# Optimization experiments

Measured on AMD Instinct MI355X. Metric: run time of the kernel, lower is better.

## Reference

```python
import jax, jax.numpy as jnp
import numpy as np

HALF_STEP = 0.05
NUM_V = 10  # clamp(floor(0.5/0.05), 2, 1000)
EPS = 1e-6


def _normalize(x):
    return x / (jnp.linalg.norm(x, axis=-1, keepdims=True) + EPS)


def _ragged_structure(edge_points_np):
    # Concrete (numpy) ragged-grid index structure: per-edge horizontal sample
    # counts from edge length, exclusive-cumsum offsets, repeat_interleave ids.
    sp = edge_points_np[:, 0]
    cd = edge_points_np[:, 1] - sp
    cl = np.linalg.norm(cd + EPS, axis=1)
    num_h = np.clip((cl // HALF_STEP).astype(np.int64), 2, 1000)  # [N]
    total_x = int(num_h.sum())
    begin = np.concatenate([[0], np.cumsum(num_h)[:-1]])           # roll-based exclusive cumsum
    eid_x = np.repeat(np.arange(len(num_h)), num_h)                # [total_x] edge id per x-sample
    pos_x = np.arange(total_x) - begin[eid_x]                      # dx integer position within edge
    eid = np.repeat(eid_x, NUM_V)                                  # [P] edge id per sample point
    pos_x_full = np.repeat(pos_x, NUM_V).astype(np.float32)        # coords_x integer part
    dy_idx = np.tile(np.arange(NUM_V), total_x).astype(np.float32) # coords_y integer part
    denom_full = np.repeat((num_h - 1)[eid_x], NUM_V).astype(np.float32)
    return (jnp.asarray(eid), jnp.asarray(pos_x_full), jnp.asarray(denom_full),
            jnp.asarray(dy_idx))


def _sample_img(img, uv):
    # img [1,3,H,W]; uv [P,2] in [0,1) -> bilinear sample (align_corners style)
    im = img[0]
    H, W = im.shape[1], im.shape[2]
    x = uv[:, 0] * (W - 1)
    y = uv[:, 1] * (H - 1)
    x0 = jnp.floor(x).astype(jnp.int32)
    y0 = jnp.floor(y).astype(jnp.int32)
    x1 = jnp.clip(x0 + 1, 0, W - 1)
    y1 = jnp.clip(y0 + 1, 0, H - 1)
    wx = (x - x0)[None]
    wy = (y - y0)[None]
    g = lambda yy, xx: im[:, yy, xx]  # [3,P] gather
    out = (g(y0, x0) * (1 - wx) * (1 - wy) + g(y0, x1) * wx * (1 - wy)
           + g(y1, x0) * (1 - wx) * wy + g(y1, x1) * wx * wy)
    return out.T  # [P,3]


def _forward(edge_points, intrinsic1, intrinsic2, extrinsic1, extrinsic2,
             rgb1, rgb2, eid, pos_x, denom, dy_idx):
    start = edge_points[:, 0]
    cur_dir = edge_points[:, 1] - start
    next_dir = edge_points[:, 3] - edge_points[:, 1]
    prev_dir = edge_points[:, 0] - edge_points[:, 2]
    cur_len = jnp.linalg.norm(cur_dir + EPS, axis=1)
    cur_dir = cur_dir / cur_len[:, None]
    cur_normal = _normalize(jnp.cross(cur_dir, next_dir))
    flip = cur_normal[:, 2] > 0  # dot with (0,0,1) > 0 -> flip sign
    cur_normal = jnp.where(flip[:, None], -cur_normal, cur_normal)
    cur_up = _normalize(jnp.cross(cur_normal, cur_dir))
    prev_normal = _normalize(jnp.cross(prev_dir, cur_dir))

    # ragged per-edge sample grid (repeat_interleave realized via gather on eid)
    coords_x = pos_x / denom * cur_len[eid]          # [P]
    coords_y = dy_idx / (NUM_V - 1) * 0.5            # [P]
    pts = (cur_dir[eid] * coords_x[:, None]
           + cur_up[eid] * coords_y[:, None]
           + start[eid])                              # [P,3]

    # view 1 projection + bilinear sample
    uv1 = pts @ intrinsic1.T
    uv1 = jnp.clip(uv1[:, :2] / uv1[:, 2:3], 0.0, 0.999999)
    s1 = _sample_img(rgb1, uv1)

    # view 2: K2_homog @ E2 @ inv(E1) applied to homogeneous points
    K2h = jnp.eye(4, dtype=pts.dtype).at[:3, :3].set(intrinsic2)
    T = K2h @ extrinsic2 @ jnp.linalg.inv(extrinsic1)
    ph = jnp.concatenate([pts, jnp.ones_like(pts[:, :1])], axis=1)
    uv2 = ph @ T.T
    uv2 = jnp.clip(uv2[:, :2] / uv2[:, 2:3], 0.0, 0.999999)
    s2 = _sample_img(rgb2, uv2)

    similarity_loss = jnp.mean((s1 - s2) ** 2)
    normal_loss = jnp.mean(1.0 - jnp.sum(cur_normal * prev_normal, axis=1)) / 2.0
    obs_normal = _normalize(jnp.cross(edge_points[:, 0], edge_points[:, 1]))
    snp = jnp.minimum(jnp.abs(jnp.sum(cur_up * obs_normal, axis=1)), 0.5)
    normalization_loss = jnp.mean(1.0 - snp / 0.5)
    return jnp.stack([similarity_loss, normal_loss, normalization_loss])


def setup_inputs() -> dict:
    key = jax.random.key(0)
    k0, k1, k2 = jax.random.split(key, 3)
    N, H, W = 10000, 1500, 2000
    # camera-space edge endpoints/neighbors, pushed in front of the camera
    edge_points = jax.random.normal(k0, (N, 4, 3), dtype=jnp.float32) \
        + jnp.array([0.0, 0.0, 6.0], dtype=jnp.float32)
    intrinsic1 = jnp.array([[0.3, 0.0, 0.5], [0.0, 0.3, 0.5], [0.0, 0.0, 1.0]],
                           dtype=jnp.float32)
    intrinsic2 = intrinsic1
    extrinsic1 = jnp.eye(4, dtype=jnp.float32)
    extrinsic2 = jnp.eye(4, dtype=jnp.float32).at[:3, 3].set(
        jnp.array([0.1, 0.0, 0.0], dtype=jnp.float32))
    rgb1 = jax.random.uniform(k1, (1, 3, H, W), dtype=jnp.float32)
    rgb2 = jax.random.uniform(k2, (1, 3, H, W), dtype=jnp.float32)
    return {"edge_points": edge_points, "intrinsic1": intrinsic1,
            "intrinsic2": intrinsic2, "extrinsic1": extrinsic1,
            "extrinsic2": extrinsic2, "rgb1": rgb1, "rgb2": rgb2}


def reference(edge_points, intrinsic1, intrinsic2, extrinsic1, extrinsic2,
              rgb1, rgb2):
    eid, pos_x, denom, dy_idx = _ragged_structure(np.asarray(edge_points))
    return _forward(edge_points, intrinsic1, intrinsic2, extrinsic1,
                    extrinsic2, rgb1, rgb2, eid, pos_x, denom, dy_idx)
```

## Files before the change

### kernel.cpp

```cpp
#include <hip/hip_runtime.h>
#include <math.h>

#define EPSF 1e-6f
#define NUM_V 10
#define W_IMG 2000
#define H_IMG 1500
#define HW_IMG (W_IMG * H_IMG)
#define TH_QUAD (H_IMG - 1)
#define SAMPLE_BLOCKS 2048
#define MAX_CHUNKS 80

__device__ __forceinline__ void cross3(const float a[3], const float b[3], float c[3]) {
    c[0] = a[1] * b[2] - a[2] * b[1];
    c[1] = a[2] * b[0] - a[0] * b[2];
    c[2] = a[0] * b[1] - a[1] * b[0];
}
__device__ __forceinline__ float dot3(const float a[3], const float b[3]) {
    return a[0] * b[0] + a[1] * b[1] + a[2] * b[2];
}
__device__ __forceinline__ float norm3(const float a[3]) {
    return sqrtf(a[0] * a[0] + a[1] * a[1] + a[2] * a[2]);
}

__device__ void do_init(const float* __restrict__ K2, const float* __restrict__ E1,
                        const float* __restrict__ E2, float* __restrict__ T) {
    double M[4][8];
    for (int i = 0; i < 4; ++i)
        for (int j = 0; j < 4; ++j) {
            M[i][j] = (double)E1[i * 4 + j];
            M[i][j + 4] = (i == j) ? 1.0 : 0.0;
        }
    for (int col = 0; col < 4; ++col) {
        int piv = col;
        double best = fabs(M[col][col]);
        for (int r = col + 1; r < 4; ++r) {
            double v = fabs(M[r][col]);
            if (v > best) { best = v; piv = r; }
        }
        if (piv != col)
            for (int j = 0; j < 8; ++j) {
                double t = M[col][j]; M[col][j] = M[piv][j]; M[piv][j] = t;
            }
        double d = M[col][col];
        for (int j = 0; j < 8; ++j) M[col][j] /= d;
        for (int r = 0; r < 4; ++r) {
            if (r == col) continue;
            double f = M[r][col];
            for (int j = 0; j < 8; ++j) M[r][j] -= f * M[col][j];
        }
    }
    double E[4][4];
    for (int i = 0; i < 4; ++i)
        for (int j = 0; j < 4; ++j) {
            double s = 0.0;
            for (int k = 0; k < 4; ++k) s += (double)E2[i * 4 + k] * M[k][j + 4];
            E[i][j] = s;
        }
    for (int i = 0; i < 4; ++i)
        for (int j = 0; j < 4; ++j) {
            double s = 0.0;
            if (i < 3) {
                for (int k = 0; k < 3; ++k) s += (double)K2[i * 3 + k] * E[k][j];
            } else {
                s = E[3][j];
            }
            T[i * 4 + j] = (float)s;
        }
}

__global__ __launch_bounds__(256) void geom_kernel(const float* __restrict__ ep, int N,
                                                   float4* __restrict__ geo,
                                                   int* __restrict__ nwv,
                                                   double* __restrict__ gnl,
                                                   double* __restrict__ gzl,
                                                   double* __restrict__ gcnt) {
    const int e = blockIdx.x * 256 + threadIdx.x;
    float nl = 0.f, zl = 0.f;
    int cn = 0;
    if (e < N) {
        const float4* P4 = (const float4*)(ep + (size_t)e * 12);
        float4 a4 = P4[0], b4 = P4[1], c4 = P4[2];
        float p0[3] = {a4.x, a4.y, a4.z};
        float p1[3] = {a4.w, b4.x, b4.y};
        float p2[3] = {b4.z, b4.w, c4.x};
        float p3[3] = {c4.y, c4.z, c4.w};
        float cd[3] = {p1[0] - p0[0], p1[1] - p0[1], p1[2] - p0[2]};
        float nd[3] = {p3[0] - p1[0], p3[1] - p1[1], p3[2] - p1[2]};
        float pd[3] = {p0[0] - p2[0], p0[1] - p2[1], p0[2] - p2[2]};
        float ce[3] = {cd[0] + EPSF, cd[1] + EPSF, cd[2] + EPSF};
        float clen = norm3(ce);
        float dir[3] = {cd[0] / clen, cd[1] / clen, cd[2] / clen};
        float cnv[3];
        cross3(dir, nd, cnv);
        float n1 = norm3(cnv) + EPSF;
        cnv[0] /= n1; cnv[1] /= n1; cnv[2] /= n1;
        if (cnv[2] > 0.f) { cnv[0] = -cnv[0]; cnv[1] = -cnv[1]; cnv[2] = -cnv[2]; }
        float up[3];
        cross3(cnv, dir, up);
        float n2 = norm3(up) + EPSF;
        up[0] /= n2; up[1] /= n2; up[2] /= n2;
        float pn[3];
        cross3(pd, dir, pn);
        float n3 = norm3(pn) + EPSF;
        pn[0] /= n3; pn[1] /= n3; pn[2] /= n3;
        float obs[3];
        cross3(p0, p1, obs);
        float n4 = norm3(obs) + EPSF;
        obs[0] /= n4; obs[1] /= n4; obs[2] /= n4;
        int nh = (int)floorf(clen / 0.05f);
        nh = max(2, min(1000, nh));
        nl = 1.f - dot3(cnv, pn);
        float snp = fminf(fabsf(dot3(up, obs)), 0.5f);
        zl = 1.f - snp * 2.f;
        int nsamp = nh * NUM_V;
        cn = nsamp;
        geo[3 * e + 0] = make_float4(p0[0], p0[1], p0[2], clen);
        geo[3 * e + 1] = make_float4(dir[0], dir[1], dir[2], (float)(nh - 1));
        geo[3 * e + 2] = make_float4(up[0], up[1], up[2], __int_as_float(nsamp));
        nwv[e] = (nsamp + 127) / 128;
    }
#pragma unroll
    for (int off = 32; off > 0; off >>= 1) {
        nl += __shfl_down(nl, off);
        zl += __shfl_down(zl, off);
        cn += __shfl_down(cn, off);
    }
    if ((threadIdx.x & 63) == 0) {
        const int w = blockIdx.x * 4 + (threadIdx.x >> 6);
        gnl[w] = (double)nl;
        gzl[w] = (double)zl;
        gcnt[w] = (double)cn;
    }
}

__global__ __launch_bounds__(256) void sched_scan_kernel(
    const int* __restrict__ nwv, int N, unsigned* __restrict__ sched, int* __restrict__ total,
    const float* __restrict__ K2, const float* __restrict__ E1, const float* __restrict__ E2,
    float* __restrict__ T) {
    __shared__ int s_red[256];
    const int b = blockIdx.x;
    const int tid = threadIdx.x;
    if (b == 0 && tid == 0) do_init(K2, E1, E2, T);
    const int lo = b * 256;
    int acc = 0;
    for (int i = tid; i < lo; i += 256) acc += nwv[i];
    s_red[tid] = acc;
    __syncthreads();
    for (int off = 128; off > 0; off >>= 1) {
        if (tid < off) s_red[tid] += s_red[tid + off];
        __syncthreads();
    }
    const int base0 = s_red[0];
    __syncthreads();
    const int e = lo + tid;
    const int mine = (e < N) ? nwv[e] : 0;
    s_red[tid] = mine;
    __syncthreads();
    for (int off = 1; off < 256; off <<= 1) {
        int v = (tid >= off) ? s_red[tid - off] : 0;
        __syncthreads();
        s_red[tid] += v;
        __syncthreads();
    }
    if (e < N) {
        int basee = base0 + (s_red[tid] - mine);
        const unsigned tag = ((unsigned)e) << 8;
        for (int j = 0; j < mine; ++j) sched[basee + j] = tag | (unsigned)j;
    }
    if (b == (int)gridDim.x - 1 && tid == 255) *total = base0 + s_red[255];
}

__device__ __forceinline__ unsigned quant565(float r, float g, float b) {
    unsigned r5 = (unsigned)fmaf(r, 31.f, 0.5f);
    unsigned g6 = (unsigned)fmaf(g, 63.f, 0.5f);
    unsigned b5 = (unsigned)fmaf(b, 31.f, 0.5f);
    return (r5 << 11) | (g6 << 5) | b5;
}

__global__ __launch_bounds__(256) void repack_quad565(const float* __restrict__ rgb1,
                                                      const float* __restrict__ rgb2,
                                                      uint2* __restrict__ t1,
                                                      uint2* __restrict__ t2) {
    const int gpi = TH_QUAD * (W_IMG / 4);
    int t = blockIdx.x * 256 + threadIdx.x;
    if (t >= 2 * gpi) return;
    const int img = t >= gpi;
    const int g = t - img * gpi;
    const int y = g / (W_IMG / 4);
    const int x = (g - y * (W_IMG / 4)) * 4;
    const float* src = img ? rgb2 : rgb1;
    uint2* dst = img ? t2 : t1;
    unsigned pk[2][5];
#pragma unroll
    for (int r = 0; r < 2; ++r) {
        const int yy = y + r;
        float px[3][5];
#pragma unroll
        for (int c = 0; c < 3; ++c) {
            const float* b = src + (size_t)c * HW_IMG + (size_t)yy * W_IMG + x;
            float4 a = *(const float4*)b;
            float e = (x + 4 < W_IMG) ? b[4] : a.w;
            px[c][0] = a.x; px[c][1] = a.y; px[c][2] = a.z; px[c][3] = a.w; px[c][4] = e;
        }
#pragma unroll
        for (int k = 0; k < 5; ++k) pk[r][k] = quant565(px[0][k], px[1][k], px[2][k]);
    }
    uint2* o = dst + (size_t)y * W_IMG + x;
#pragma unroll
    for (int k = 0; k < 4; ++k)
        o[k] = make_uint2(pk[0][k] | (pk[0][k + 1] << 16), pk[1][k] | (pk[1][k + 1] << 16));
}

__device__ __forceinline__ float mse565(uint2 qa, uint2 qb, float wxa, float wya, float wxb,
                                        float wyb) {
    float wa00 = (1.f - wxa) * (1.f - wya), wa01 = wxa * (1.f - wya);
    float wa10 = (1.f - wxa) * wya, wa11 = wxa * wya;
    float wb00 = (1.f - wxb) * (1.f - wyb), wb01 = wxb * (1.f - wyb);
    float wb10 = (1.f - wxb) * wyb, wb11 = wxb * wyb;
    unsigned a00 = qa.x & 0xffffu, a01 = qa.x >> 16, a10 = qa.y & 0xffffu, a11 = qa.y >> 16;
    unsigned b00 = qb.x & 0xffffu, b01 = qb.x >> 16, b10 = qb.y & 0xffffu, b11 = qb.y >> 16;
    float ra = fmaf((float)(a00 >> 11), wa00, fmaf((float)(a01 >> 11), wa01,
               fmaf((float)(a10 >> 11), wa10, (float)(a11 >> 11) * wa11)));
    float rb = fmaf((float)(b00 >> 11), wb00, fmaf((float)(b01 >> 11), wb01,
               fmaf((float)(b10 >> 11), wb10, (float)(b11 >> 11) * wb11)));
    float ga = fmaf((float)((a00 >> 5) & 63u), wa00, fmaf((float)((a01 >> 5) & 63u), wa01,
               fmaf((float)((a10 >> 5) & 63u), wa10, (float)((a11 >> 5) & 63u) * wa11)));
    float gb = fmaf((float)((b00 >> 5) & 63u), wb00, fmaf((float)((b01 >> 5) & 63u), wb01,
               fmaf((float)((b10 >> 5) & 63u), wb10, (float)((b11 >> 5) & 63u) * wb11)));
    float ba = fmaf((float)(a00 & 31u), wa00, fmaf((float)(a01 & 31u), wa01,
               fmaf((float)(a10 & 31u), wa10, (float)(a11 & 31u) * wa11)));
    float bb = fmaf((float)(b00 & 31u), wb00, fmaf((float)(b01 & 31u), wb01,
               fmaf((float)(b10 & 31u), wb10, (float)(b11 & 31u) * wb11)));
    float dr = (ra - rb) * (1.f / 31.f);
    float dg = (ga - gb) * (1.f / 63.f);
    float db = (ba - bb) * (1.f / 31.f);
    return fmaf(dr, dr, fmaf(dg, dg, db * db));
}

__global__ __launch_bounds__(256) void sample_kernel(
    const float4* __restrict__ geo, const float* __restrict__ K1, const float* __restrict__ T,
    const uint2* __restrict__ im1, const uint2* __restrict__ im2,
    const unsigned* __restrict__ sched, const int* __restrict__ total_p,
    double* __restrict__ part) {
    const int wid = blockIdx.x * 4 + (threadIdx.x >> 6);
    const int lane = threadIdx.x & 63;
    const int nw = gridDim.x * 4;
    const int total = *total_p;

    const float k00 = K1[0], k01 = K1[1], k02 = K1[2];
    const float k10 = K1[3], k11 = K1[4], k12 = K1[5];
    const float k20 = K1[6], k21 = K1[7], k22 = K1[8];
    const float t00 = T[0], t01 = T[1], t02 = T[2], t03 = T[3];
    const float t10 = T[4], t11 = T[5], t12 = T[6], t13 = T[7];
    const float t20 = T[8], t21 = T[9], t22 = T[10], t23 = T[11];

    float lsum = 0.f;
    for (int base = wid; base < total; base += 2 * nw) {
        const int idxB = base + nw;
        const bool has2 = idxB < total;
        const unsigned sA = (unsigned)__builtin_amdgcn_readfirstlane((int)sched[base]);
        const unsigned sB =
            has2 ? (unsigned)__builtin_amdgcn_readfirstlane((int)sched[idxB]) : sA;
        const int eA = (int)(sA >> 8), kA = (int)(sA & 255u);
        const int eB = (int)(sB >> 8), kB = (int)(sB & 255u);
        const float4 a0 = geo[3 * eA + 0], a1 = geo[3 * eA + 1], a2 = geo[3 * eA + 2];
        const float4 b0 = geo[3 * eB + 0], b1 = geo[3 * eB + 1], b2 = geo[3 * eB + 2];
        const int nsA = __float_as_int(a2.w), nsB = __float_as_int(b2.w);
        const float lodA = a0.w * __builtin_amdgcn_rcpf(a1.w);
        const float lodB = b0.w * __builtin_amdgcn_rcpf(b1.w);

        int off1[4], off2[4];
        float wx1[4], wy1[4], wx2[4], wy2[4];
        bool ok[4];
#pragma unroll
        for (int j = 0; j < 4; ++j) {
            const int d = j >> 1, h = j & 1;
            const float4 g0 = d ? b0 : a0;
            const float4 g1 = d ? b1 : a1;
            const float4 g2 = d ? b2 : a2;
            const int ns = d ? nsB : nsA;
            const int kk = d ? kB : kA;
            const float lod = d ? lodB : lodA;
            const int i = kk * 128 + h * 64 + lane;
            ok[j] = (i < ns) && (d == 0 || has2);
            const int ic = min(i, ns - 1);
            int px = ic / NUM_V;
            int dy = ic - px * NUM_V;
            float cx = (float)px * lod;
            float cy = (float)dy * (0.5f / 9.0f);
            float X = fmaf(g1.x, cx, fmaf(g2.x, cy, g0.x));
            float Y = fmaf(g1.y, cx, fmaf(g2.y, cy, g0.y));
            float Z = fmaf(g1.z, cx, fmaf(g2.z, cy, g0.z));
            float iw1 = __builtin_amdgcn_rcpf(fmaf(k20, X, fmaf(k21, Y, k22 * Z)));
            float u1 = fminf(fmaxf(fmaf(k00, X, fmaf(k01, Y, k02 * Z)) * iw1, 0.f), 0.999999f);
            float v1 = fminf(fmaxf(fmaf(k10, X, fmaf(k11, Y, k12 * Z)) * iw1, 0.f), 0.999999f);
            float iw2 = __builtin_amdgcn_rcpf(fmaf(t20, X, fmaf(t21, Y, fmaf(t22, Z, t23))));
            float u2 = fminf(
                fmaxf(fmaf(t00, X, fmaf(t01, Y, fmaf(t02, Z, t03))) * iw2, 0.f), 0.999999f);
            float v2 = fminf(
                fmaxf(fmaf(t10, X, fmaf(t11, Y, fmaf(t12, Z, t13))) * iw2, 0.f), 0.999999f);
            float xa = u1 * (float)(W_IMG - 1), ya = v1 * (float)(H_IMG - 1);
            float xb = u2 * (float)(W_IMG - 1), yb = v2 * (float)(H_IMG - 1);
            float fxa = floorf(xa), fya = floorf(ya), fxb = floorf(xb), fyb = floorf(yb);
            off1[j] = (int)fya * W_IMG + (int)fxa;
            off2[j] = (int)fyb * W_IMG + (int)fxb;
            wx1[j] = xa - fxa; wy1[j] = ya - fya;
            wx2[j] = xb - fxb; wy2[j] = yb - fyb;
        }
        uint2 q1[4], q2[4];
#pragma unroll
        for (int j = 0; j < 4; ++j) q1[j] = im1[off1[j]];
#pragma unroll
        for (int j = 0; j < 4; ++j) q2[j] = im2[off2[j]];
#pragma unroll
        for (int j = 0; j < 4; ++j) {
            float v = mse565(q1[j], q2[j], wx1[j], wy1[j], wx2[j], wy2[j]);
            lsum += ok[j] ? v : 0.f;
        }
    }
    double dsum = (double)lsum;
#pragma unroll
    for (int off = 32; off > 0; off >>= 1) dsum += __shfl_down(dsum, off);
    if (lane == 0) part[wid] = dsum;
}

__global__ __launch_bounds__(256) void finalize_kernel(const double* __restrict__ part, int NP,
                                                       const double* __restrict__ gnl,
                                                       const double* __restrict__ gzl,
                                                       const double* __restrict__ gcnt, int N,
                                                       int NW, float* __restrict__ out) {
    __shared__ double s_s[4], s_a[4], s_b[4], s_c[4];
    double s = 0.0, a = 0.0, b = 0.0, c = 0.0;
    for (int i = threadIdx.x; i < NP; i += 256) s += part[i];
    for (int i = threadIdx.x; i < NW; i += 256) {
        a += gnl[i];
        b += gzl[i];
        c += gcnt[i];
    }
#pragma unroll
    for (int off = 32; off > 0; off >>= 1) {
        s += __shfl_down(s, off);
        a += __shfl_down(a, off);
        b += __shfl_down(b, off);
        c += __shfl_down(c, off);
    }
    const int wave = threadIdx.x >> 6;
    if ((threadIdx.x & 63) == 0) {
        s_s[wave] = s; s_a[wave] = a; s_b[wave] = b; s_c[wave] = c;
    }
    __syncthreads();
    if (threadIdx.x == 0) {
        double S = s_s[0] + s_s[1] + s_s[2] + s_s[3];
        double A = s_a[0] + s_a[1] + s_a[2] + s_a[3];
        double B = s_b[0] + s_b[1] + s_b[2] + s_b[3];
        double C = s_c[0] + s_c[1] + s_c[2] + s_c[3];
        out[0] = (float)(S / (C * 3.0));
        out[1] = (float)(A / (double)N * 0.5);
        out[2] = (float)(B / (double)N);
    }
}

extern "C" void kernel_launch(void* const* d_in, const int* in_sizes, int n_in, void* d_out,
                              int out_size, void* d_ws, size_t ws_size, hipStream_t stream) {
    const float* ep = (const float*)d_in[0];
    const float* K1 = (const float*)d_in[1];
    const float* K2 = (const float*)d_in[2];
    const float* E1 = (const float*)d_in[3];
    const float* E2 = (const float*)d_in[4];
    const float* rgb1 = (const float*)d_in[5];
    const float* rgb2 = (const float*)d_in[6];
    float* out = (float*)d_out;
    const int N = in_sizes[0] / 12;

    const int GB = (N + 255) / 256;
    const int NW = GB * 4;
    const int NPART = SAMPLE_BLOCKS * 4;

    char* p = (char*)d_ws;
    auto align256 = [](char* q) { return (char*)(((size_t)q + 255) & ~(size_t)255); };
    float* T = (float*)p;                 p += 256;
    int* total = (int*)p;                 p += 256;
    float4* geo = (float4*)p;             p += (size_t)3 * N * sizeof(float4);
    p = align256(p);
    int* nwv = (int*)p;                   p += (size_t)N * sizeof(int);
    p = align256(p);
    double* part = (double*)p;            p += (size_t)NPART * sizeof(double);
    double* gnl = (double*)p;             p += (size_t)NW * sizeof(double);
    double* gzl = (double*)p;             p += (size_t)NW * sizeof(double);
    double* gcnt = (double*)p;            p += (size_t)NW * sizeof(double);
    p = align256(p);
    unsigned* sched = (unsigned*)p;       p += (size_t)N * MAX_CHUNKS * sizeof(unsigned);
    p = align256(p);
    uint2* img1 = (uint2*)p;
    uint2* img2 = img1 + (size_t)TH_QUAD * W_IMG;

    geom_kernel<<<GB, 256, 0, stream>>>(ep, N, geo, nwv, gnl, gzl, gcnt);
    sched_scan_kernel<<<GB, 256, 0, stream>>>(nwv, N, sched, total, K2, E1, E2, T);
    const int rp_threads = 2 * TH_QUAD * (W_IMG / 4);
    repack_quad565<<<(rp_threads + 255) / 256, 256, 0, stream>>>(rgb1, rgb2, img1, img2);
    sample_kernel<<<SAMPLE_BLOCKS, 256, 0, stream>>>(geo, K1, T, img1, img2, sched, total, part);
    finalize_kernel<<<1, 256, 0, stream>>>(part, NPART, gnl, gzl, gcnt, N, NW, out);
}
```

Baseline: 184.6 us.

## Repack only image rows covered by projected edge bounding box

Adds an init kernel that computes the camera transform and resets a row bounding box. The geometry kernel projects each edge's sampling rectangle corners into both images and reduces min/max rows with atomics. The repack kernel then skips rows outside that range, avoiding quantizing unused image rows, and writes output as wider uint4 stores. This costs one extra launch and atomics, and relies on the corner projection plus margin bounding all bilinear taps, which may fail if the projection is non-monotonic or crosses depth sign.

```diff
diff --git a/kernel.cpp b/kernel.cpp
--- a/kernel.cpp
+++ b/kernel.cpp
@@ -9,6 +9,7 @@
 #define TH_QUAD (H_IMG - 1)
 #define SAMPLE_BLOCKS 2048
 #define MAX_CHUNKS 80
+#define ROW_MARGIN 8
 
 __device__ __forceinline__ void cross3(const float a[3], const float b[3], float c[3]) {
     c[0] = a[1] * b[2] - a[2] * b[1];
@@ -68,15 +69,31 @@
         }
 }
 
+__global__ void init_kernel(const float* __restrict__ K2, const float* __restrict__ E1,
+                            const float* __restrict__ E2, float* __restrict__ T,
+                            int* __restrict__ bbox) {
+    if (threadIdx.x != 0) return;
+    do_init(K2, E1, E2, T);
+    bbox[0] = 0x7fffffff;
+    bbox[1] = -0x7fffffff;
+    bbox[2] = 0x7fffffff;
+    bbox[3] = -0x7fffffff;
+}
+
 __global__ __launch_bounds__(256) void geom_kernel(const float* __restrict__ ep, int N,
+                                                   const float* __restrict__ K1,
+                                                   const float* __restrict__ T,
                                                    float4* __restrict__ geo,
                                                    int* __restrict__ nwv,
                                                    double* __restrict__ gnl,
                                                    double* __restrict__ gzl,
-                                                   double* __restrict__ gcnt) {
+                                                   double* __restrict__ gcnt,
+                                                   int* __restrict__ bbox) {
     const int e = blockIdx.x * 256 + threadIdx.x;
     float nl = 0.f, zl = 0.f;
     int cn = 0;
+    int r1min = 0x7fffffff, r1max = -0x7fffffff;
+    int r2min = 0x7fffffff, r2max = -0x7fffffff;
     if (e < N) {
         const float4* P4 = (const float4*)(ep + (size_t)e * 12);
         float4 a4 = P4[0], b4 = P4[1], c4 = P4[2];
@@ -118,29 +135,71 @@
         geo[3 * e + 1] = make_float4(dir[0], dir[1], dir[2], (float)(nh - 1));
         geo[3 * e + 2] = make_float4(up[0], up[1], up[2], __int_as_float(nsamp));
         nwv[e] = (nsamp + 127) / 128;
+
+        const float k10 = K1[3], k11 = K1[4], k12 = K1[5];
+        const float k20 = K1[6], k21 = K1[7], k22 = K1[8];
+        const float t10 = T[4], t11 = T[5], t12 = T[6], t13 = T[7];
+        const float t20 = T[8], t21 = T[9], t22 = T[10], t23 = T[11];
+        float v1min = 1e9f, v1max = -1e9f, v2min = 1e9f, v2max = -1e9f;
+#pragma unroll
+        for (int c = 0; c < 4; ++c) {
+            float cx = (c & 1) ? clen : 0.f;
+            float cy = (c & 2) ? 0.5f : 0.f;
+            float X = fmaf(dir[0], cx, fmaf(up[0], cy, p0[0]));
+            float Y = fmaf(dir[1], cx, fmaf(up[1], cy, p0[1]));
+            float Z = fmaf(dir[2], cx, fmaf(up[2], cy, p0[2]));
+            float iw1 = __builtin_amdgcn_rcpf(fmaf(k20, X, fmaf(k21, Y, k22 * Z)));
+            float v1 = fminf(fmaxf(fmaf(k10, X, fmaf(k11, Y, k12 * Z)) * iw1, 0.f), 0.999999f);
+            float iw2 = __builtin_amdgcn_rcpf(fmaf(t20, X, fmaf(t21, Y, fmaf(t22, Z, t23))));
+            float v2 = fminf(
+                fmaxf(fmaf(t10, X, fmaf(t11, Y, fmaf(t12, Z, t13))) * iw2, 0.f), 0.999999f);
+            v1min = fminf(v1min, v1); v1max = fmaxf(v1max, v1);
+            v2min = fminf(v2min, v2); v2max = fmaxf(v2max, v2);
+        }
+        r1min = (int)floorf(v1min * (float)(H_IMG - 1)) - ROW_MARGIN;
+        r1max = (int)floorf(v1max * (float)(H_IMG - 1)) + ROW_MARGIN;
+        r2min = (int)floorf(v2min * (float)(H_IMG - 1)) - ROW_MARGIN;
+        r2max = (int)floorf(v2max * (float)(H_IMG - 1)) + ROW_MARGIN;
     }
 #pragma unroll
     for (int off = 32; off > 0; off >>= 1) {
         nl += __shfl_down(nl, off);
         zl += __shfl_down(zl, off);
         cn += __shfl_down(cn, off);
-    }
+        r1min = min(r1min, __shfl_down(r1min, off));
+        r1max = max(r1max, __shfl_down(r1max, off));
+        r2min = min(r2min, __shfl_down(r2min, off));
+        r2max = max(r2max, __shfl_down(r2max, off));
+    }
+    __shared__ int s_bb[4][4];
+    const int wave = threadIdx.x >> 6;
     if ((threadIdx.x & 63) == 0) {
-        const int w = blockIdx.x * 4 + (threadIdx.x >> 6);
+        const int w = blockIdx.x * 4 + wave;
         gnl[w] = (double)nl;
         gzl[w] = (double)zl;
         gcnt[w] = (double)cn;
-    }
-}
-
-__global__ __launch_bounds__(256) void sched_scan_kernel(
-    const int* __restrict__ nwv, int N, unsigned* __restrict__ sched, int* __restrict__ total,
-    const float* __restrict__ K2, const float* __restrict__ E1, const float* __restrict__ E2,
-    float* __restrict__ T) {
+        s_bb[wave][0] = r1min; s_bb[wave][1] = r1max;
+        s_bb[wave][2] = r2min; s_bb[wave][3] = r2max;
+    }
+    __syncthreads();
+    if (threadIdx.x == 0) {
+        int m0 = min(min(s_bb[0][0], s_bb[1][0]), min(s_bb[2][0], s_bb[3][0]));
+        int m1 = max(max(s_bb[0][1], s_bb[1][1]), max(s_bb[2][1], s_bb[3][1]));
+        int m2 = min(min(s_bb[0][2], s_bb[1][2]), min(s_bb[2][2], s_bb[3][2]));
+        int m3 = max(max(s_bb[0][3], s_bb[1][3]), max(s_bb[2][3], s_bb[3][3]));
+        atomicMin(&bbox[0], m0);
+        atomicMax(&bbox[1], m1);
+        atomicMin(&bbox[2], m2);
+        atomicMax(&bbox[3], m3);
+    }
+}
+
+__global__ __launch_bounds__(256) void sched_scan_kernel(const int* __restrict__ nwv, int N,
+                                                         unsigned* __restrict__ sched,
+                                                         int* __restrict__ total) {
     __shared__ int s_red[256];
     const int b = blockIdx.x;
     const int tid = threadIdx.x;
-    if (b == 0 && tid == 0) do_init(K2, E1, E2, T);
     const int lo = b * 256;
     int acc = 0;
     for (int i = tid; i < lo; i += 256) acc += nwv[i];
@@ -180,13 +239,17 @@
 __global__ __launch_bounds__(256) void repack_quad565(const float* __restrict__ rgb1,
                                                       const float* __restrict__ rgb2,
                                                       uint2* __restrict__ t1,
-                                                      uint2* __restrict__ t2) {
+                                                      uint2* __restrict__ t2,
+                                                      const int* __restrict__ bbox) {
     const int gpi = TH_QUAD * (W_IMG / 4);
     int t = blockIdx.x * 256 + threadIdx.x;
     if (t >= 2 * gpi) return;
     const int img = t >= gpi;
     const int g = t - img * gpi;
     const int y = g / (W_IMG / 4);
+    const int bmin = max(0, bbox[img * 2]);
+    const int bmax = min(TH_QUAD - 1, bbox[img * 2 + 1]);
+    if (y < bmin || y > bmax) return;
     const int x = (g - y * (W_IMG / 4)) * 4;
     const float* src = img ? rgb2 : rgb1;
     uint2* dst = img ? t2 : t1;
@@ -206,9 +269,12 @@
         for (int k = 0; k < 5; ++k) pk[r][k] = quant565(px[0][k], px[1][k], px[2][k]);
     }
     uint2* o = dst + (size_t)y * W_IMG + x;
-#pragma unroll
-    for (int k = 0; k < 4; ++k)
-        o[k] = make_uint2(pk[0][k] | (pk[0][k + 1] << 16), pk[1][k] | (pk[1][k + 1] << 16));
+    uint4 s0 = make_uint4(pk[0][0] | (pk[0][1] << 16), pk[1][0] | (pk[1][1] << 16),
+                          pk[0][1] | (pk[0][2] << 16), pk[1][1] | (pk[1][2] << 16));
+    uint4 s1 = make_uint4(pk[0][2] | (pk[0][3] << 16), pk[1][2] | (pk[1][3] << 16),
+                          pk[0][3] | (pk[0][4] << 16), pk[1][3] | (pk[1][4] << 16));
+    *(uint4*)(o + 0) = s0;
+    *(uint4*)(o + 2) = s1;
 }
 
 __device__ __forceinline__ float mse565(uint2 qa, uint2 qb, float wxa, float wya, float wxb,
@@ -379,7 +445,8 @@
     char* p = (char*)d_ws;
     auto align256 = [](char* q) { return (char*)(((size_t)q + 255) & ~(size_t)255); };
     float* T = (float*)p;                 p += 256;
-    int* total = (int*)p;                 p += 256;
+    int* total = (int*)p;                 p += 128;
+    int* bbox = (int*)p;                  p += 128;
     float4* geo = (float4*)p;             p += (size_t)3 * N * sizeof(float4);
     p = align256(p);
     int* nwv = (int*)p;                   p += (size_t)N * sizeof(int);
@@ -394,10 +461,11 @@
     uint2* img1 = (uint2*)p;
     uint2* img2 = img1 + (size_t)TH_QUAD * W_IMG;
 
-    geom_kernel<<<GB, 256, 0, stream>>>(ep, N, geo, nwv, gnl, gzl, gcnt);
-    sched_scan_kernel<<<GB, 256, 0, stream>>>(nwv, N, sched, total, K2, E1, E2, T);
+    init_kernel<<<1, 64, 0, stream>>>(K2, E1, E2, T, bbox);
+    geom_kernel<<<GB, 256, 0, stream>>>(ep, N, K1, T, geo, nwv, gnl, gzl, gcnt, bbox);
+    sched_scan_kernel<<<GB, 256, 0, stream>>>(nwv, N, sched, total);
     const int rp_threads = 2 * TH_QUAD * (W_IMG / 4);
-    repack_quad565<<<(rp_threads + 255) / 256, 256, 0, stream>>>(rgb1, rgb2, img1, img2);
+    repack_quad565<<<(rp_threads + 255) / 256, 256, 0, stream>>>(rgb1, rgb2, img1, img2, bbox);
     sample_kernel<<<SAMPLE_BLOCKS, 256, 0, stream>>>(geo, K1, T, img1, img2, sched, total, part);
     finalize_kernel<<<1, 256, 0, stream>>>(part, NPART, gnl, gzl, gcnt, N, NW, out);
 }
```

Measured after the change: 177.6 us. 1.04x faster.
